# Optimization experiments

Hardware: AMD Instinct MI355X
Metric: run time of the kernel (lower is better)

Reference implementation:

```python
import jax, jax.numpy as jnp
import numpy as np

N = 65536   # total sentences (ragged axis)
B = 4096    # bags
D = 2304    # filter_num * piece = 768 * 3
C = 53      # class_num (NYT-10 relations)


def setup_inputs() -> dict:
    key = jax.random.key(0)
    k1, k2, k3, k4 = jax.random.split(key, 4)
    reps = jax.random.normal(k1, (N, D), dtype=jnp.float32)
    # strictly increasing bag boundaries (no empty bags), endpoints 0 and N
    rng = np.random.default_rng(0)
    inner = np.sort(rng.choice(np.arange(1, N), size=B - 1, replace=False))
    scope = jnp.asarray(np.concatenate([[0], inner, [N]]), dtype=jnp.int32)
    label = jax.random.randint(k2, (B,), 0, C, dtype=jnp.int32)
    W = jax.random.normal(k3, (C, D), dtype=jnp.float32) / np.float32(np.sqrt(D))
    b = jax.random.normal(k4, (C,), dtype=jnp.float32) * 0.01
    return {"reps": reps, "scope": scope, "label": label, "W": W, "b": b}


def reference(reps, scope, label, W, b):
    # dropout omitted (inference-deterministic reference); dense + softmax over ALL
    # sentences at once instead of the per-bag python loop
    logits = jnp.einsum('nd,cd->nc', reps, W) + b          # [N, C]
    probs = jax.nn.softmax(logits, axis=-1)                 # [N, C]
    sent_idx = jnp.arange(N)
    # bag id per sentence: largest i with scope[i] <= j
    seg = jnp.searchsorted(scope, sent_idx, side='right') - 1   # [N]
    # training-branch MIL selection: per bag, pick the sentence whose prob at the
    # bag label is maximal (first such sentence, matching torch.max semantics)
    lp = probs[sent_idx, label[seg]]                        # [N]
    seg_max = jax.ops.segment_max(lp, seg, num_segments=B)  # [B]
    cand = jnp.where(lp >= seg_max[seg], sent_idx, N)
    sel = jnp.clip(jax.ops.segment_min(cand, seg, num_segments=B), 0, N - 1)  # [B]
    return probs[sel]                                       # [B, C]
```

## Files before the change

### kernel.cpp

```cpp
#include <hip/hip_runtime.h>
#include <cstdint>
#include <cstddef>

#define N_SENT 65536
#define DIMS   2304
#define NBAG   4096
#define NCLS   53
#define CPAD   64
#define PROW   56


__device__ __forceinline__ void async_copy16(const float* g, float* l) {
    __builtin_amdgcn_global_load_lds(
        (const __attribute__((address_space(1))) unsigned int*)g,
        (__attribute__((address_space(3))) unsigned int*)l,
        16, 0, 0);
}

__global__ void prep_kernel(const float* __restrict__ W,
                            const int* __restrict__ scope,
                            const int* __restrict__ label,
                            float* __restrict__ Wt,
                            int* __restrict__ tcls) {
    int gid = blockIdx.x * 256 + threadIdx.x;
    if (blockIdx.x < (DIMS * CPAD) / 256) {
        int k = gid >> 6;
        int c = gid & 63;
        Wt[gid] = (c < NCLS) ? W[(size_t)c * DIMS + k] : 0.0f;
    } else {
        int bag = gid - (DIMS * CPAD);
        if (bag < NBAG) {
            int s = scope[bag], e = scope[bag + 1];
            int lb = label[bag];
            for (int j = s; j < e; ++j) tcls[j] = lb;
        }
    }
}

__launch_bounds__(256, 2)
__global__ void logits_kernel(const float* __restrict__ reps,
                              const float* __restrict__ Wt,
                              const float* __restrict__ bias_g,
                              const int* __restrict__ tcls,
                              float* __restrict__ probs,
                              float* __restrict__ lp) {
    __shared__ float sA[128 * 64];
    __shared__ float sW[64 * CPAD];

    const int tid  = threadIdx.x;
    const int ct   = tid & 15;
    const int mt   = tid >> 4;
    const int wave = tid >> 6;
    const int lane = tid & 63;
    const int m0   = blockIdx.x * 128;

    float acc[8][4];
#pragma unroll
    for (int i = 0; i < 8; ++i)
#pragma unroll
        for (int c = 0; c < 4; ++c) acc[i][c] = 0.0f;

    const int r_in = lane >> 4;
    const int jj   = lane & 15;

    for (int kc = 0; kc < DIMS; kc += 64) {
#pragma unroll
        for (int s = 0; s < 8; ++s) {
            int r  = (wave * 8 + s) * 4 + r_in;
            int gk = kc + (((jj - (r & 15)) * 4) & 63);
            const float* gptr = reps + (size_t)(m0 + r) * DIMS + gk;
            float* lptr = sA + (wave * 8 + s) * 256;
            async_copy16(gptr, lptr);
        }
#pragma unroll
        for (int s = 0; s < 4; ++s) {
            const float* gptr = Wt + (size_t)kc * CPAD + (wave * 4 + s) * 256 + lane * 4;
            float* lptr = sW + (wave * 4 + s) * 256;
            async_copy16(gptr, lptr);
        }
        __syncthreads();

        for (int kk = 0; kk < 64; kk += 4) {
            float4 wv[4];
#pragma unroll
            for (int j = 0; j < 4; ++j)
                wv[j] = *(const float4*)&sW[(kk + j) * CPAD + 4 * ct];
            const int col = (kk + 4 * mt) & 63;
#pragma unroll
            for (int i = 0; i < 8; ++i) {
                float4 rv = *(const float4*)&sA[(mt + 16 * i) * 64 + col];
                const float rk[4] = {rv.x, rv.y, rv.z, rv.w};
#pragma unroll
                for (int j = 0; j < 4; ++j) {
                    const float* wj = (const float*)&wv[j];
#pragma unroll
                    for (int c = 0; c < 4; ++c)
                        acc[i][c] = fmaf(rk[j], wj[c], acc[i][c]);
                }
            }
        }
        __syncthreads();
    }

    float bv[4];
    bool  valid[4];
#pragma unroll
    for (int c = 0; c < 4; ++c) {
        int cc = 4 * ct + c;
        valid[c] = (cc < NCLS);
        bv[c] = valid[c] ? bias_g[cc] : 0.0f;
    }

#pragma unroll
    for (int i = 0; i < 8; ++i) {
        int m = m0 + mt + 16 * i;
        float l[4];
        float mx = -1e30f;
#pragma unroll
        for (int c = 0; c < 4; ++c) {
            l[c] = valid[c] ? (acc[i][c] + bv[c]) : -1e30f;
            mx = fmaxf(mx, l[c]);
        }
#pragma unroll
        for (int off = 1; off < 16; off <<= 1)
            mx = fmaxf(mx, __shfl_xor(mx, off, 16));
        float e[4];
        float s = 0.0f;
#pragma unroll
        for (int c = 0; c < 4; ++c) {
            e[c] = valid[c] ? __expf(l[c] - mx) : 0.0f;
            s += e[c];
        }
#pragma unroll
        for (int off = 1; off < 16; off <<= 1)
            s += __shfl_xor(s, off, 16);
        float inv = 1.0f / s;

        float4 pv = make_float4(e[0] * inv, e[1] * inv, e[2] * inv, e[3] * inv);
        float* prow = probs + (size_t)m * PROW;
        if (ct < 13)       *(float4*)(prow + 4 * ct) = pv;
        else if (ct == 13) prow[52] = pv.x;

        int t = tcls[m];
        if ((t >> 2) == ct) {
            const float* pe = (const float*)&pv;
            lp[m] = pe[t & 3];
        }
    }
}

__global__ void select_kernel(const int* __restrict__ scope,
                              const float* __restrict__ lp,
                              const float* __restrict__ probs,
                              float* __restrict__ out) {
    int wave = threadIdx.x >> 6;
    int lane = threadIdx.x & 63;
    int bag  = blockIdx.x * 4 + wave;
    int s = scope[bag], e = scope[bag + 1];

    float bvv = -1e38f;
    int   bj  = 0x7fffffff;
    for (int j = s + lane; j < e; j += 64) {
        float v = lp[j];
        if (v > bvv) { bvv = v; bj = j; }
    }
#pragma unroll
    for (int off = 1; off < 64; off <<= 1) {
        float ov = __shfl_xor(bvv, off, 64);
        int   oj = __shfl_xor(bj, off, 64);
        if (ov > bvv || (ov == bvv && oj < bj)) { bvv = ov; bj = oj; }
    }
    if (lane < NCLS)
        out[(size_t)bag * NCLS + lane] = probs[(size_t)bj * PROW + lane];
}

extern "C" void kernel_launch(void* const* d_in, const int* in_sizes, int n_in,
                              void* d_out, int out_size, void* d_ws, size_t ws_size,
                              hipStream_t stream) {
    const float* reps  = (const float*)d_in[0];
    const int*   scope = (const int*)d_in[1];
    const int*   label = (const int*)d_in[2];
    const float* W     = (const float*)d_in[3];
    const float* b     = (const float*)d_in[4];
    float*       out   = (float*)d_out;

    char* ws = (char*)d_ws;
    float* Wt    = (float*)(ws);
    float* probs = (float*)(ws + 589824);
    float* lp    = (float*)(ws + 589824 + 14680064);
    int*   tcls  = (int*)(ws + 589824 + 14680064 + 262144);

    prep_kernel<<<592, 256, 0, stream>>>(W, scope, label, Wt, tcls);
    logits_kernel<<<512, 256, 0, stream>>>(reps, Wt, b, tcls, probs, lp);
    select_kernel<<<NBAG / 4, 256, 0, stream>>>(scope, lp, probs, out);
}
```

Before: 871.0 us.

## Restructure logits GEMM with per-wave class slices and double-buffered LDS staging

Rewrites the logits kernel so each of 8 waves owns an 8-class slice of W, read as wave-uniform vector loads straight from global memory instead of staging W in LDS. Each thread accumulates 4 rows × 8 classes. The reps tile is double-buffered in LDS with async loads, so the next k-slice loads while the current one computes. Softmax now reduces across waves through LDS, and the bias is prepadded with -inf in prep. Blocks double to 512 threads and 256 rows, which halves the grid to 256 blocks and may reduce occupancy and latency hiding.

Result: slower. 1.084 ms (+24.5%).

```diff
diff --git a/kernel.cpp b/kernel.cpp
--- a/kernel.cpp
+++ b/kernel.cpp
@@ -6,8 +6,9 @@
 #define DIMS   2304
 #define NBAG   4096
 #define NCLS   53
-#define CPAD   64
 #define PROW   56
+
+typedef __attribute__((ext_vector_type(8))) float f32x8;
 
 
 __device__ __forceinline__ void async_copy16(const float* g, float* l) {
@@ -20,131 +21,158 @@
 __global__ void prep_kernel(const float* __restrict__ W,
                             const int* __restrict__ scope,
                             const int* __restrict__ label,
-                            float* __restrict__ Wt,
-                            int* __restrict__ tcls) {
+                            const float* __restrict__ b,
+                            float* __restrict__ Wcs,
+                            int* __restrict__ tcls,
+                            float* __restrict__ bias64) {
     int gid = blockIdx.x * 256 + threadIdx.x;
-    if (blockIdx.x < (DIMS * CPAD) / 256) {
-        int k = gid >> 6;
-        int c = gid & 63;
-        Wt[gid] = (c < NCLS) ? W[(size_t)c * DIMS + k] : 0.0f;
+    if (gid < 8 * DIMS * 8) {
+        int w = gid / (DIMS * 8);
+        int r = gid % (DIMS * 8);
+        int k = r >> 3;
+        int c = r & 7;
+        int cls = 8 * w + c;
+        Wcs[gid] = (cls < NCLS) ? W[(size_t)cls * DIMS + k] : 0.0f;
     } else {
-        int bag = gid - (DIMS * CPAD);
-        if (bag < NBAG) {
-            int s = scope[bag], e = scope[bag + 1];
-            int lb = label[bag];
+        int id = gid - 8 * DIMS * 8;
+        if (id < NBAG) {
+            int s = scope[id], e = scope[id + 1];
+            int lb = label[id];
             for (int j = s; j < e; ++j) tcls[j] = lb;
-        }
-    }
-}
-
-__launch_bounds__(256, 2)
+        } else if (id < NBAG + 64) {
+            int c = id - NBAG;
+            bias64[c] = (c < NCLS) ? b[c] : -1e30f;
+        }
+    }
+}
+
+__launch_bounds__(512, 2)
 __global__ void logits_kernel(const float* __restrict__ reps,
-                              const float* __restrict__ Wt,
-                              const float* __restrict__ bias_g,
+                              const float* __restrict__ Wcs,
+                              const float* __restrict__ bias64,
                               const int* __restrict__ tcls,
                               float* __restrict__ probs,
                               float* __restrict__ lp) {
-    __shared__ float sA[128 * 64];
-    __shared__ float sW[64 * CPAD];
-
-    const int tid  = threadIdx.x;
-    const int ct   = tid & 15;
-    const int mt   = tid >> 4;
-    const int wave = tid >> 6;
-    const int lane = tid & 63;
-    const int m0   = blockIdx.x * 128;
-
-    float acc[8][4];
-#pragma unroll
-    for (int i = 0; i < 8; ++i)
-#pragma unroll
-        for (int c = 0; c < 4; ++c) acc[i][c] = 0.0f;
-
-    const int r_in = lane >> 4;
-    const int jj   = lane & 15;
-
-    for (int kc = 0; kc < DIMS; kc += 64) {
-#pragma unroll
-        for (int s = 0; s < 8; ++s) {
-            int r  = (wave * 8 + s) * 4 + r_in;
-            int gk = kc + (((jj - (r & 15)) * 4) & 63);
-            const float* gptr = reps + (size_t)(m0 + r) * DIMS + gk;
-            float* lptr = sA + (wave * 8 + s) * 256;
-            async_copy16(gptr, lptr);
-        }
+    __shared__ float lds[2][8192];
+
+    const int tid = threadIdx.x;
+    const int L   = tid & 63;
+    const int w   = __builtin_amdgcn_readfirstlane(tid >> 6);
+    const int m0  = blockIdx.x * 256;
+
+    float acc[4][8];
+#pragma unroll
+    for (int i = 0; i < 4; ++i)
+#pragma unroll
+        for (int c = 0; c < 8; ++c) acc[i][c] = 0.0f;
+
+    const float* wbase = Wcs + (size_t)w * DIMS * 8;
+
+    auto stage = [&](int t, int buf) {
 #pragma unroll
         for (int s = 0; s < 4; ++s) {
-            const float* gptr = Wt + (size_t)kc * CPAD + (wave * 4 + s) * 256 + lane * 4;
-            float* lptr = sW + (wave * 4 + s) * 256;
-            async_copy16(gptr, lptr);
-        }
+            int id = w * 4 + s;
+            int q  = id >> 3;
+            int c4 = id & 7;
+            const float* g = reps + (size_t)(m0 + q * 64 + L) * DIMS + t * 32 + c4 * 4;
+            float* l = &lds[buf][c4 * 1024 + q * 256];
+            async_copy16(g, l);
+        }
+    };
+
+    stage(0, 0);
+
+    for (int t = 0; t < 72; ++t) {
         __syncthreads();
-
-        for (int kk = 0; kk < 64; kk += 4) {
-            float4 wv[4];
-#pragma unroll
-            for (int j = 0; j < 4; ++j)
-                wv[j] = *(const float4*)&sW[(kk + j) * CPAD + 4 * ct];
-            const int col = (kk + 4 * mt) & 63;
-#pragma unroll
-            for (int i = 0; i < 8; ++i) {
-                float4 rv = *(const float4*)&sA[(mt + 16 * i) * 64 + col];
-                const float rk[4] = {rv.x, rv.y, rv.z, rv.w};
-#pragma unroll
-                for (int j = 0; j < 4; ++j) {
-                    const float* wj = (const float*)&wv[j];
-#pragma unroll
-                    for (int c = 0; c < 4; ++c)
-                        acc[i][c] = fmaf(rk[j], wj[c], acc[i][c]);
+        if (t + 1 < 72) stage(t + 1, (t + 1) & 1);
+        const float* lb = lds[t & 1];
+        const float* wk = wbase + (size_t)t * 32 * 8;
+#pragma unroll
+        for (int kk = 0; kk < 32; kk += 4) {
+            f32x8 wv0 = *(const f32x8*)(wk + (kk + 0) * 8);
+            f32x8 wv1 = *(const f32x8*)(wk + (kk + 1) * 8);
+            f32x8 wv2 = *(const f32x8*)(wk + (kk + 2) * 8);
+            f32x8 wv3 = *(const f32x8*)(wk + (kk + 3) * 8);
+            const float* slab = lb + (kk >> 2) * 1024;
+#pragma unroll
+            for (int i = 0; i < 4; ++i) {
+                float4 rv = *(const float4*)&slab[(L + 64 * i) * 4];
+#pragma unroll
+                for (int c = 0; c < 8; ++c) {
+                    acc[i][c] = fmaf(rv.x, wv0[c], acc[i][c]);
+                    acc[i][c] = fmaf(rv.y, wv1[c], acc[i][c]);
+                    acc[i][c] = fmaf(rv.z, wv2[c], acc[i][c]);
+                    acc[i][c] = fmaf(rv.w, wv3[c], acc[i][c]);
                 }
             }
         }
-        __syncthreads();
-    }
-
-    float bv[4];
-    bool  valid[4];
-#pragma unroll
-    for (int c = 0; c < 4; ++c) {
-        int cc = 4 * ct + c;
-        valid[c] = (cc < NCLS);
-        bv[c] = valid[c] ? bias_g[cc] : 0.0f;
-    }
-
-#pragma unroll
-    for (int i = 0; i < 8; ++i) {
-        int m = m0 + mt + 16 * i;
-        float l[4];
-        float mx = -1e30f;
-#pragma unroll
-        for (int c = 0; c < 4; ++c) {
-            l[c] = valid[c] ? (acc[i][c] + bv[c]) : -1e30f;
-            mx = fmaxf(mx, l[c]);
-        }
-#pragma unroll
-        for (int off = 1; off < 16; off <<= 1)
-            mx = fmaxf(mx, __shfl_xor(mx, off, 16));
-        float e[4];
+    }
+
+    __syncthreads();
+    float* red = &lds[0][0];
+
+    f32x8 bv = *(const f32x8*)(bias64 + 8 * w);
+
+    float mx[4];
+#pragma unroll
+    for (int i = 0; i < 4; ++i) {
+        float pm = -1e38f;
+#pragma unroll
+        for (int c = 0; c < 8; ++c) {
+            acc[i][c] += bv[c];
+            pm = fmaxf(pm, acc[i][c]);
+        }
+        red[(L + 64 * i) * 8 + w] = pm;
+    }
+    __syncthreads();
+#pragma unroll
+    for (int i = 0; i < 4; ++i) {
+        const float* r8 = &red[(L + 64 * i) * 8];
+        float m01 = fmaxf(r8[0], r8[1]), m23 = fmaxf(r8[2], r8[3]);
+        float m45 = fmaxf(r8[4], r8[5]), m67 = fmaxf(r8[6], r8[7]);
+        mx[i] = fmaxf(fmaxf(m01, m23), fmaxf(m45, m67));
+    }
+    __syncthreads();
+    float ps[4];
+#pragma unroll
+    for (int i = 0; i < 4; ++i) {
         float s = 0.0f;
 #pragma unroll
-        for (int c = 0; c < 4; ++c) {
-            e[c] = valid[c] ? __expf(l[c] - mx) : 0.0f;
-            s += e[c];
-        }
-#pragma unroll
-        for (int off = 1; off < 16; off <<= 1)
-            s += __shfl_xor(s, off, 16);
+        for (int c = 0; c < 8; ++c) {
+            acc[i][c] = __expf(acc[i][c] - mx[i]);
+            s += acc[i][c];
+        }
+        red[(L + 64 * i) * 8 + w] = s;
+    }
+    __syncthreads();
+#pragma unroll
+    for (int i = 0; i < 4; ++i) {
+        const float* r8 = &red[(L + 64 * i) * 8];
+        float s = ((r8[0] + r8[1]) + (r8[2] + r8[3])) + ((r8[4] + r8[5]) + (r8[6] + r8[7]));
         float inv = 1.0f / s;
-
-        float4 pv = make_float4(e[0] * inv, e[1] * inv, e[2] * inv, e[3] * inv);
+        int m = m0 + L + 64 * i;
         float* prow = probs + (size_t)m * PROW;
-        if (ct < 13)       *(float4*)(prow + 4 * ct) = pv;
-        else if (ct == 13) prow[52] = pv.x;
-
-        int t = tcls[m];
-        if ((t >> 2) == ct) {
-            const float* pe = (const float*)&pv;
-            lp[m] = pe[t & 3];
+        float4 p0 = make_float4(acc[i][0] * inv, acc[i][1] * inv, acc[i][2] * inv, acc[i][3] * inv);
+        float4 p1 = make_float4(acc[i][4] * inv, acc[i][5] * inv, acc[i][6] * inv, acc[i][7] * inv);
+        if (w < 6) {
+            *(float4*)(prow + 8 * w)     = p0;
+            *(float4*)(prow + 8 * w + 4) = p1;
+        } else if (w == 6) {
+            *(float4*)(prow + 48) = p0;
+            prow[52] = p1.x;
+        }
+        int tlab = tcls[m];
+        if ((tlab >> 3) == w) {
+            int c = tlab & 7;
+            float v = acc[i][0];
+            v = (c == 1) ? acc[i][1] : v;
+            v = (c == 2) ? acc[i][2] : v;
+            v = (c == 3) ? acc[i][3] : v;
+            v = (c == 4) ? acc[i][4] : v;
+            v = (c == 5) ? acc[i][5] : v;
+            v = (c == 6) ? acc[i][6] : v;
+            v = (c == 7) ? acc[i][7] : v;
+            lp[m] = v * inv;
         }
     }
 }
@@ -185,12 +213,13 @@
     float*       out   = (float*)d_out;
 
     char* ws = (char*)d_ws;
-    float* Wt    = (float*)(ws);
-    float* probs = (float*)(ws + 589824);
-    float* lp    = (float*)(ws + 589824 + 14680064);
-    int*   tcls  = (int*)(ws + 589824 + 14680064 + 262144);
-
-    prep_kernel<<<592, 256, 0, stream>>>(W, scope, label, Wt, tcls);
-    logits_kernel<<<512, 256, 0, stream>>>(reps, Wt, b, tcls, probs, lp);
+    float* Wcs    = (float*)(ws);
+    float* probs  = (float*)(ws + 589824);
+    float* lp     = (float*)(ws + 589824 + 14680064);
+    int*   tcls   = (int*)(ws + 589824 + 14680064 + 262144);
+    float* bias64 = (float*)(ws + 589824 + 14680064 + 262144 + 262144);
+
+    prep_kernel<<<593, 256, 0, stream>>>(W, scope, label, b, Wcs, tcls, bias64);
+    logits_kernel<<<256, 512, 0, stream>>>(reps, Wcs, bias64, tcls, probs, lp);
     select_kernel<<<NBAG / 4, 256, 0, stream>>>(scope, lp, probs, out);
 }
```
